# Optimization experiments

Measured on AMD Instinct MI355X. Metric: run time of the kernel, lower is better.

The kernel has to match this reference:

```python
import jax, jax.numpy as jnp
import numpy as np

N, E, C, L = 50000, 625000, 128, 4
H = 2 * C  # hidden size of per-layer ObjectModel
FRAC_SCALE = 1.0 / 16.0   # fractional_bitwidth = 4
Q_MAX = 8.0               # int_bitwidth = 4 -> signed fixed point range [-8, 8 - 1/16]


def fq(x):
    """Fixed-point fake-quantize (4 int bits, 4 frac bits, signed)."""
    return jnp.clip(jnp.round(x / FRAC_SCALE) * FRAC_SCALE, -Q_MAX, Q_MAX - FRAC_SCALE)


def qlin(h, W, b):
    # QuantLinear: input/weight/bias/output all quantized
    return fq(fq(h) @ fq(W) + fq(b))


def qbn(h, w, b):
    # BatchNorm1dToQuantScaleBias in inference: per-channel scale + bias
    return fq(fq(h) * fq(w) + fq(b))


def setup_inputs() -> dict:
    key = jax.random.key(0)
    ks = jax.random.split(key, 24)
    d = {}
    d["x"] = jax.random.normal(ks[0], (N, 3), dtype=jnp.float32)
    d["edge_attr"] = jax.random.normal(ks[1], (E, 4), dtype=jnp.float32)
    d["edge_index"] = jax.random.randint(ks[2], (2, E), 0, N, dtype=jnp.int64)
    # encoders
    d["node_W"] = jax.random.normal(ks[3], (3, C), dtype=jnp.float32) * 0.4
    d["node_b"] = jax.random.normal(ks[4], (C,), dtype=jnp.float32) * 0.2
    d["edge_W"] = jax.random.normal(ks[5], (4, C), dtype=jnp.float32) * 0.4
    d["edge_b"] = jax.random.normal(ks[6], (C,), dtype=jnp.float32) * 0.2
    d["node_bn_w"] = 1.0 + 0.1 * jax.random.normal(ks[7], (C,), dtype=jnp.float32)
    d["node_bn_b"] = 0.1 * jax.random.normal(ks[8], (C,), dtype=jnp.float32)
    d["edge_bn_w"] = 1.0 + 0.1 * jax.random.normal(ks[9], (C,), dtype=jnp.float32)
    d["edge_bn_b"] = 0.1 * jax.random.normal(ks[10], (C,), dtype=jnp.float32)
    # per-layer ObjectModel params (stacked over L)
    d["W1"] = jax.random.normal(ks[11], (L, C, H), dtype=jnp.float32) * (0.5 / np.sqrt(C))
    d["b1"] = jax.random.normal(ks[12], (L, H), dtype=jnp.float32) * 0.1
    d["bn_w"] = 1.0 + 0.1 * jax.random.normal(ks[13], (L, H), dtype=jnp.float32)
    d["bn_b"] = 0.1 * jax.random.normal(ks[14], (L, H), dtype=jnp.float32)
    d["W2"] = jax.random.normal(ks[15], (L, H, C), dtype=jnp.float32) * (0.5 / np.sqrt(H))
    d["b2"] = jax.random.normal(ks[16], (L, C), dtype=jnp.float32) * 0.1
    d["fc_W"] = jax.random.normal(ks[17], (C, 1), dtype=jnp.float32) * (0.5 / np.sqrt(C))
    d["fc_b"] = jax.random.normal(ks[18], (1,), dtype=jnp.float32) * 0.1
    return d


def reference(x, edge_attr, edge_index, node_W, node_b, edge_W, edge_b,
              node_bn_w, node_bn_b, edge_bn_w, edge_bn_b,
              W1, b1, bn_w, bn_b, W2, b2, fc_W, fc_b):
    src = edge_index[0]  # x_j (source) under flow='source_to_target'
    tgt = edge_index[1]  # aggregation target i

    h = fq(qlin(x, node_W, node_b))            # node encoder [N, C]
    e = fq(qlin(edge_attr, edge_W, edge_b))    # edge encoder [E, C]
    h = qbn(h, node_bn_w, node_bn_b)
    e = qbn(e, edge_bn_w, edge_bn_b)

    for l in range(L):
        # message: quant(x_j) + quant(edge_attr), QuantReLU
        msg = fq(jax.nn.relu(fq(h[src]) + fq(e)))          # [E, C]
        agg = jax.ops.segment_sum(msg, tgt, num_segments=N)  # scatter-sum [N, C]
        u = fq(agg)
        # ObjectModel: QuantLinear -> ScaleBias BN -> QuantReLU -> QuantLinear, then QuantIdentity
        z = qlin(u, W1[l], b1[l])
        z = qbn(z, bn_w[l], bn_b[l])
        z = fq(jax.nn.relu(z))
        z = fq(qlin(z, W2[l], b2[l]))
        h = h + z                                           # residual

    pooled = jnp.mean(h, axis=0, keepdims=True)  # global_mean_pool, batch=None -> [1, C]
    out = qlin(fq(pooled), fc_W, fc_b)           # [1, 1]
    out = fq(jax.nn.sigmoid(fq(out)))            # QuantSigmoid
    return out.reshape(-1)                       # [1]
```

## Files before the change

kernel.cpp:

```cpp
#include <hip/hip_runtime.h>
#include <stdint.h>

#define NN 50000
#define EE 625000
#define EPAD (EE + 16)
#define CC 128
#define HH 256
#define LL 4
#define NPAD 50048
#define NBLK (NPAD/64)
#define R2 32

typedef __attribute__((ext_vector_type(4))) int   i32x4;

__device__ __forceinline__ float qbf(float x){
  return fminf(127.f, fmaxf(-128.f, rintf(x*16.f)));
}
__device__ __forceinline__ float rq16(float t){
  return fminf(127.f, fmaxf(-128.f, rintf(t*0.0625f)));
}
__device__ __forceinline__ int rne16c(int t){
  int q = (t + 7 + ((t>>4)&1)) >> 4;
  return min(max(q, -128), 127);
}
__device__ __forceinline__ int dot4b(int q, int w, int c){
#if __has_builtin(__builtin_amdgcn_sdot4)
  return __builtin_amdgcn_sdot4(q, w, c, false);
#else
  int s = c;
  #pragma unroll
  for (int i=0;i<4;++i)
    s += ((int)(signed char)((q >> (8*i)) & 0xff)) *
         ((int)(signed char)((w >> (8*i)) & 0xff));
  return s;
#endif
}

__global__ void k_qbig(const float* __restrict__ W1, const float* __restrict__ W2,
                       signed char* __restrict__ w1q8, signed char* __restrict__ w2q8){
  int i = blockIdx.x*256 + threadIdx.x;
  if (i >= LL*CC*HH) return;
  {
    float v = qbf(W1[i]);
    int l = i / (CC*HH); int r = i - l*CC*HH; int c = r / HH; int hh = r - c*HH;
    w1q8[((size_t)l*HH + hh)*CC + c] = (signed char)v;
  }
  {
    float v = qbf(W2[i]);
    int l = i / (HH*CC); int r = i - l*HH*CC; int hh = r / CC; int c = r - hh*CC;
    w2q8[((size_t)l*CC + c)*HH + hh] = (signed char)v;
  }
}

struct QS { const float* s; float* d; int n; float m; };
struct QSArgs { QS q[10]; };

__global__ void k_qsmall(QSArgs a){
  for (int r=0;r<10;++r){
    QS qs = a.q[r];
    for (int i = blockIdx.x*blockDim.x + threadIdx.x; i < qs.n; i += gridDim.x*blockDim.x)
      qs.d[i] = qs.m * qbf(qs.s[i]);
  }
}

__global__ void k_epki(const float* __restrict__ eW, const float* __restrict__ eb,
                       const float* __restrict__ bnw, const float* __restrict__ bnb,
                       int4* __restrict__ epk){
  int c = threadIdx.x;
  int w0 = (int)qbf(eW[c])      & 0xff;
  int w1 = (int)qbf(eW[CC+c])   & 0xff;
  int w2 = (int)qbf(eW[2*CC+c]) & 0xff;
  int w3 = (int)qbf(eW[3*CC+c]) & 0xff;
  epk[c] = make_int4(w0 | (w1<<8) | (w2<<16) | (w3<<24),
                     16 * (int)qbf(eb[c]),
                     (int)qbf(bnw[c]),
                     16 * (int)qbf(bnb[c]));
}

__global__ __launch_bounds__(256) void k_node_enc(
    const float* __restrict__ x, const float* __restrict__ nW,
    const float* __restrict__ nb16, const float* __restrict__ bnw,
    const float* __restrict__ bnb16, short* __restrict__ h0,
    signed char* __restrict__ hq8){
  int idx = blockIdx.x*256 + threadIdx.x;
  int n = idx >> 7, c = idx & 127;
  float x0 = qbf(x[n*3]), x1 = qbf(x[n*3+1]), x2 = qbf(x[n*3+2]);
  float S = x0*nW[c] + x1*nW[CC+c] + x2*nW[2*CC+c];
  float v1 = rq16(S + nb16[c]);
  float v2 = rq16(v1*bnw[c] + bnb16[c]);
  h0[idx] = (short)v2;
  hq8[idx] = (signed char)v2;
}

__global__ void k_deg(const int* __restrict__ ei, int* __restrict__ deg){
  int e = blockIdx.x*256 + threadIdx.x;
  if (e < EE) atomicAdd(&deg[ei[EE + e]], 1);
}

__global__ __launch_bounds__(256) void k_scanA(const int* __restrict__ deg,
                                               int* __restrict__ offI,
                                               int* __restrict__ btot){
  __shared__ int sh[256];
  int t = threadIdx.x;
  int base = blockIdx.x*1024 + t*4;
  int v[4]; int s = 0;
  #pragma unroll
  for (int i=0;i<4;++i){ v[i] = (base+i < NN) ? deg[base+i] : 0; s += v[i]; }
  sh[t] = s; __syncthreads();
  for (int off=1; off<256; off<<=1){
    int xv = (t>=off) ? sh[t-off] : 0;
    __syncthreads();
    sh[t] += xv;
    __syncthreads();
  }
  int run = (t>0) ? sh[t-1] : 0;
  #pragma unroll
  for (int i=0;i<4;++i){ run += v[i]; if (base+i < NN) offI[base+i] = run; }
  if (t==255) btot[blockIdx.x] = sh[255];
}

__global__ void k_scanB(const int* __restrict__ btot, int* __restrict__ boff, int nblk){
  if (threadIdx.x==0 && blockIdx.x==0){
    int run = 0;
    for (int b=0;b<nblk;++b){ int v = btot[b]; boff[b] = run; run += v; }
  }
}

__global__ void k_scanC(const int* __restrict__ boff, const int* __restrict__ deg,
                        int* __restrict__ offI, int* __restrict__ cursor){
  int i = blockIdx.x*256 + threadIdx.x;
  if (i < NN){
    int v = offI[i] + boff[i>>10];
    offI[i] = v;
    cursor[i] = v - deg[i];
  }
}

__global__ void k_fill(const int* __restrict__ ei, const float* __restrict__ ea,
                       int* __restrict__ cursor, int2* __restrict__ adjq){
  int e = blockIdx.x*256 + threadIdx.x;
  if (e < EE){
    int tgt = ei[EE + e];
    int p = atomicAdd(&cursor[tgt], 1);
    float4 v = ((const float4*)ea)[e];
    int b0 = (int)qbf(v.x) & 0xff, b1 = (int)qbf(v.y) & 0xff;
    int b2 = (int)qbf(v.z) & 0xff, b3 = (int)qbf(v.w) & 0xff;
    adjq[p] = make_int2(ei[e] * CC, b0 | (b1<<8) | (b2<<16) | (b3<<24));
  }
}

__global__ __launch_bounds__(256) void k_msg(
    const int* __restrict__ offI, const int* __restrict__ deg_,
    const int2* __restrict__ adjq, const int4* __restrict__ epk,
    const signed char* __restrict__ hq8, signed char* __restrict__ uq){
  int n = blockIdx.x*4 + (threadIdx.x >> 6);
  int lane = threadIdx.x & 63;
  int c0 = lane*2;
  int4 P0 = epk[c0];
  int4 P1 = epk[c0+1];
  int end = offI[n];
  int start = end - deg_[n];
  int acc0 = 0, acc1 = 0;
  for (int base = start; base < end; base += 16){
    int rem = end - base;
    int2 a = adjq[base + min(lane, rem-1)];
    ushort hv[16]; int qk[16];
    #pragma unroll
    for (int j=0;j<16;++j){
      int soj = __builtin_amdgcn_readlane(a.x, j);
      hv[j] = *(const ushort*)(hq8 + soj + c0);
      qk[j] = __builtin_amdgcn_readlane(a.y, j);
    }
    #pragma unroll
    for (int j=0;j<16;++j){
      if (j < rem){
        int h0 = ((int)hv[j] << 24) >> 24;
        int h1 = ((int)(short)hv[j]) >> 8;
        int q = qk[j];
        int v10 = rne16c(dot4b(q, P0.x, P0.y));
        int v11 = rne16c(dot4b(q, P1.x, P1.y));
        int e0 = rne16c(v10*P0.z + P0.w);
        int e1 = rne16c(v11*P1.z + P1.w);
        acc0 += min(max(h0 + e0, 0), 127);
        acc1 += min(max(h1 + e1, 0), 127);
      }
    }
  }
  int ua = min(acc0, 127), ub = min(acc1, 127);
  *(ushort*)(uq + (size_t)n*CC + c0) = (ushort)((ua & 0xff) | ((ub & 0xff) << 8));
}

__global__ __launch_bounds__(256, 3) void k_om(
    int l, const signed char* __restrict__ uq,
    const signed char* __restrict__ w1q8, const float* __restrict__ b1q16,
    const float* __restrict__ bnwf, const float* __restrict__ bnb16,
    const signed char* __restrict__ w2q8, const float* __restrict__ b2q16,
    const short* __restrict__ h_in, short* __restrict__ h_out,
    signed char* __restrict__ hq8, int* __restrict__ partial){
  __shared__ signed char uL[64][144];
  __shared__ signed char zL[64][272];
  int t = threadIdx.x;
  int nb = blockIdx.x * 64;
  {
    const i32x4* src = (const i32x4*)(uq + (size_t)nb*CC + t*32);
    int flat = t*32; int r = flat >> 7, c = flat & 127;
    *(i32x4*)&uL[r][c]      = src[0];
    *(i32x4*)&uL[r][c + 16] = src[1];
  }
  int lane = t & 63, wv = t >> 6;
  int lr = lane & 15, lk = lane >> 4;
  const signed char* W1p = w1q8 + (size_t)l*HH*CC;
  i32x4 w1f[2][4];
  #pragma unroll
  for (int ks=0; ks<2; ++ks)
    #pragma unroll
    for (int ci=0; ci<4; ++ci)
      w1f[ks][ci] = *(const i32x4*)(W1p + (size_t)(wv*64 + ci*16 + lr)*CC + ks*64 + lk*16);
  __syncthreads();

  i32x4 acc[4][4];
  #pragma unroll
  for (int mi=0;mi<4;++mi)
    #pragma unroll
    for (int ci=0;ci<4;++ci) acc[mi][ci] = (i32x4){0,0,0,0};
  #pragma unroll
  for (int ks=0; ks<2; ++ks){
    i32x4 av[4];
    #pragma unroll
    for (int mi=0;mi<4;++mi) av[mi] = *(const i32x4*)&uL[mi*16+lr][ks*64 + lk*16];
    #pragma unroll
    for (int mi=0;mi<4;++mi)
      #pragma unroll
      for (int ci=0;ci<4;++ci)
        acc[mi][ci] = __builtin_amdgcn_mfma_i32_16x16x64_i8(av[mi], w1f[ks][ci], acc[mi][ci], 0,0,0);
  }
  #pragma unroll
  for (int ci=0;ci<4;++ci){
    int hcol = wv*64 + ci*16 + lr;
    float b1 = b1q16[l*HH + hcol];
    float bw = bnwf[l*HH + hcol];
    float bb = bnb16[l*HH + hcol];
    #pragma unroll
    for (int mi=0;mi<4;++mi){
      #pragma unroll
      for (int r=0;r<4;++r){
        float v1 = rq16((float)acc[mi][ci][r] + b1);
        float v2 = fmaxf(rq16(v1*bw + bb), 0.f);
        zL[mi*16 + lk*4 + r][hcol] = (signed char)v2;
      }
    }
  }
  const signed char* W2p = w2q8 + (size_t)l*CC*HH;
  i32x4 w2f[4][2];
  #pragma unroll
  for (int ks=0; ks<4; ++ks)
    #pragma unroll
    for (int ci=0; ci<2; ++ci)
      w2f[ks][ci] = *(const i32x4*)(W2p + (size_t)(wv*32 + ci*16 + lr)*HH + ks*64 + lk*16);
  __syncthreads();

  i32x4 a2[4][2];
  #pragma unroll
  for (int mi=0;mi<4;++mi){ a2[mi][0] = (i32x4){0,0,0,0}; a2[mi][1] = (i32x4){0,0,0,0}; }
  #pragma unroll
  for (int ks=0; ks<4; ++ks){
    i32x4 av[4];
    #pragma unroll
    for (int mi=0;mi<4;++mi) av[mi] = *(const i32x4*)&zL[mi*16+lr][ks*64 + lk*16];
    #pragma unroll
    for (int mi=0;mi<4;++mi)
      #pragma unroll
      for (int ci=0;ci<2;++ci)
        a2[mi][ci] = __builtin_amdgcn_mfma_i32_16x16x64_i8(av[mi], w2f[ks][ci], a2[mi][ci], 0,0,0);
  }
  int psum[2] = {0, 0};
  #pragma unroll
  for (int ci=0;ci<2;++ci){
    int ccol = wv*32 + ci*16 + lr;
    float b2 = b2q16[l*CC + ccol];
    #pragma unroll
    for (int mi=0;mi<4;++mi){
      #pragma unroll
      for (int r=0;r<4;++r){
        int node = nb + mi*16 + lk*4 + r;
        float v = rq16((float)a2[mi][ci][r] + b2);
        int hn = (int)h_in[(size_t)node*CC + ccol] + (int)v;
        if (node < NN){
          h_out[(size_t)node*CC + ccol] = (short)hn;
          hq8[(size_t)node*CC + ccol] = (signed char)min(max(hn, -128), 127);
          psum[ci] += hn;
        }
      }
    }
  }
  if (partial){
    #pragma unroll
    for (int ci=0;ci<2;++ci){
      int s = psum[ci];
      s += __shfl_xor(s, 16);
      s += __shfl_xor(s, 32);
      if (lk == 0)
        partial[blockIdx.x*CC + wv*32 + ci*16 + lr] = s;
    }
  }
}

__global__ __launch_bounds__(256) void k_red(
    const int* __restrict__ partial, int* __restrict__ partial2){
  int t = threadIdx.x;
  int c = t & 127;
  int sub = blockIdx.x*2 + (t >> 7);
  int s = 0;
  for (int b = sub; b < NBLK; b += R2) s += partial[b*CC + c];
  partial2[sub*CC + c] = s;
}

__global__ __launch_bounds__(256) void k_final(
    const int* __restrict__ partial2, const float* __restrict__ fcwf,
    const float* __restrict__ fcb16, float* __restrict__ out){
  __shared__ int ired[128];
  __shared__ float red[128];
  int t = threadIdx.x;
  int c = t & 127, half = t >> 7;
  int s = 0;
  #pragma unroll
  for (int b = half; b < R2; b += 2) s += partial2[b*CC + c];
  if (half) ired[c] = s;
  __syncthreads();
  if (!half){
    int sc = s + ired[c];
    double m = (double)sc / (double)NN;
    float pq = fminf(127.f, fmaxf(-128.f, (float)rint(m)));
    red[c] = pq * fcwf[c];
  }
  __syncthreads();
  for (int o=64;o>0;o>>=1){ if (t<o) red[t] += red[t+o]; __syncthreads(); }
  if (t==0){
    float v = rq16(red[0] + fcb16[0]);
    float o1 = v * 0.0625f;
    float sg = 1.f/(1.f + expf(-o1));
    float oq = fminf(127.f, fmaxf(-128.f, rintf(sg*16.f)));
    out[0] = oq * 0.0625f;
  }
}

extern "C" void kernel_launch(void* const* d_in, const int* in_sizes, int n_in,
                              void* d_out, int out_size, void* d_ws, size_t ws_size,
                              hipStream_t stream){
  (void)in_sizes; (void)n_in; (void)out_size; (void)ws_size;
  const float* x   = (const float*)d_in[0];
  const float* ea  = (const float*)d_in[1];
  const int*   ei  = (const int*)d_in[2];
  const float* W1  = (const float*)d_in[11];
  const float* W2  = (const float*)d_in[15];

  char* w = (char*)d_ws;
  auto alloc = [&](size_t bytes)->char*{
    char* p = w; w += (bytes + 255) & ~(size_t)255; return p;
  };
  short* h0        = (short*)alloc((size_t)NPAD*CC*2);
  short* h1        = (short*)alloc((size_t)NPAD*CC*2);
  signed char* hq8 = (signed char*)alloc((size_t)NPAD*CC);
  signed char* uq  = (signed char*)alloc((size_t)NPAD*CC);
  int2* adjq       = (int2*)alloc((size_t)EPAD*8);
  int* deg         = (int*)alloc(NN*4);
  int* offI        = (int*)alloc(NN*4);
  int* cursor      = (int*)alloc(NN*4);
  int* btot        = (int*)alloc(64*4);
  int* boff        = (int*)alloc(64*4);
  int* partial     = (int*)alloc((size_t)NBLK*CC*4);
  int* partial2    = (int*)alloc((size_t)R2*CC*4);
  signed char* w1q8= (signed char*)alloc((size_t)LL*CC*HH);
  signed char* w2q8= (signed char*)alloc((size_t)LL*CC*HH);
  float* nodeWf    = (float*)alloc(3*CC*4);
  float* nb16f     = (float*)alloc(CC*4);
  float* nbnwf     = (float*)alloc(CC*4);
  float* nbnb16f   = (float*)alloc(CC*4);
  float* b1q16f    = (float*)alloc(LL*HH*4);
  float* bnwf      = (float*)alloc(LL*HH*4);
  float* bnb16f    = (float*)alloc(LL*HH*4);
  float* b2q16f    = (float*)alloc(LL*CC*4);
  float* fcwf      = (float*)alloc(CC*4);
  float* fcb16f    = (float*)alloc(256);
  int4* epk        = (int4*)alloc(CC*16);

  hipMemsetAsync(deg, 0, NN*4, stream);

  k_qbig<<<(LL*CC*HH + 255)/256, 256, 0, stream>>>(W1, W2, w1q8, w2q8);

  QSArgs qa;
  auto setq = [&](int r, int idx, float* d, int n, float m){
    qa.q[r].s = (const float*)d_in[idx]; qa.q[r].d = d; qa.q[r].n = n; qa.q[r].m = m;
  };
  setq(0, 3,  nodeWf,  3*CC, 1.f);
  setq(1, 4,  nb16f,   CC,   16.f);
  setq(2, 7,  nbnwf,   CC,   1.f);
  setq(3, 8,  nbnb16f, CC,   16.f);
  setq(4, 12, b1q16f,  LL*HH, 16.f);
  setq(5, 13, bnwf,    LL*HH, 1.f);
  setq(6, 14, bnb16f,  LL*HH, 16.f);
  setq(7, 16, b2q16f,  LL*CC, 16.f);
  setq(8, 17, fcwf,    CC,   1.f);
  setq(9, 18, fcb16f,  1,    16.f);
  k_qsmall<<<4, 256, 0, stream>>>(qa);
  k_epki<<<1, 128, 0, stream>>>((const float*)d_in[5], (const float*)d_in[6],
                                (const float*)d_in[9], (const float*)d_in[10], epk);

  k_node_enc<<<(NN*CC)/256, 256, 0, stream>>>(x, nodeWf, nb16f, nbnwf, nbnb16f, h0, hq8);
  k_deg<<<(EE+255)/256, 256, 0, stream>>>(ei, deg);
  int nblk = (NN + 1023)/1024;
  k_scanA<<<nblk, 256, 0, stream>>>(deg, offI, btot);
  k_scanB<<<1, 64, 0, stream>>>(btot, boff, nblk);
  k_scanC<<<(NN+255)/256, 256, 0, stream>>>(boff, deg, offI, cursor);
  k_fill<<<(EE+255)/256, 256, 0, stream>>>(ei, ea, cursor, adjq);

  for (int l=0;l<LL;++l){
    const short* hi = (l & 1) ? h1 : h0;
    short* ho       = (l & 1) ? h0 : h1;
    k_msg<<<NN/4, 256, 0, stream>>>(offI, deg, adjq, epk, hq8, uq);
    k_om<<<NBLK, 256, 0, stream>>>(l, uq, w1q8, b1q16f, bnwf, bnb16f,
                                   w2q8, b2q16f, hi, ho, hq8,
                                   (l == LL-1) ? partial : nullptr);
  }
  k_red<<<R2/2, 256, 0, stream>>>(partial, partial2);
  k_final<<<1, 256, 0, stream>>>(partial2, fcwf, fcb16f, (float*)d_out);
}
```

Before: 380.3 us.

## Fuse message aggregation into per-layer object-model kernel via shared memory

Merges the gather/scatter message kernel into the MLP kernel so each 64-node block aggregates its own nodes' messages directly into shared memory, removing the intermediate uq buffer and one launch per layer. The quantized node features are double-buffered so blocks can read the previous layer's values while writing new ones. The tradeoff is far fewer waves doing the latency-bound edge gather, each processing 16 nodes serially, which may reduce memory-level parallelism.

```diff
diff --git a/kernel.cpp b/kernel.cpp
--- a/kernel.cpp
+++ b/kernel.cpp
@@ -149,66 +149,23 @@
   }
 }
 
-__global__ __launch_bounds__(256) void k_msg(
+__global__ __launch_bounds__(256, 3) void k_layer(
+    int l,
     const int* __restrict__ offI, const int* __restrict__ deg_,
     const int2* __restrict__ adjq, const int4* __restrict__ epk,
-    const signed char* __restrict__ hq8, signed char* __restrict__ uq){
-  int n = blockIdx.x*4 + (threadIdx.x >> 6);
-  int lane = threadIdx.x & 63;
-  int c0 = lane*2;
-  int4 P0 = epk[c0];
-  int4 P1 = epk[c0+1];
-  int end = offI[n];
-  int start = end - deg_[n];
-  int acc0 = 0, acc1 = 0;
-  for (int base = start; base < end; base += 16){
-    int rem = end - base;
-    int2 a = adjq[base + min(lane, rem-1)];
-    ushort hv[16]; int qk[16];
-    #pragma unroll
-    for (int j=0;j<16;++j){
-      int soj = __builtin_amdgcn_readlane(a.x, j);
-      hv[j] = *(const ushort*)(hq8 + soj + c0);
-      qk[j] = __builtin_amdgcn_readlane(a.y, j);
-    }
-    #pragma unroll
-    for (int j=0;j<16;++j){
-      if (j < rem){
-        int h0 = ((int)hv[j] << 24) >> 24;
-        int h1 = ((int)(short)hv[j]) >> 8;
-        int q = qk[j];
-        int v10 = rne16c(dot4b(q, P0.x, P0.y));
-        int v11 = rne16c(dot4b(q, P1.x, P1.y));
-        int e0 = rne16c(v10*P0.z + P0.w);
-        int e1 = rne16c(v11*P1.z + P1.w);
-        acc0 += min(max(h0 + e0, 0), 127);
-        acc1 += min(max(h1 + e1, 0), 127);
-      }
-    }
-  }
-  int ua = min(acc0, 127), ub = min(acc1, 127);
-  *(ushort*)(uq + (size_t)n*CC + c0) = (ushort)((ua & 0xff) | ((ub & 0xff) << 8));
-}
-
-__global__ __launch_bounds__(256, 3) void k_om(
-    int l, const signed char* __restrict__ uq,
     const signed char* __restrict__ w1q8, const float* __restrict__ b1q16,
     const float* __restrict__ bnwf, const float* __restrict__ bnb16,
     const signed char* __restrict__ w2q8, const float* __restrict__ b2q16,
     const short* __restrict__ h_in, short* __restrict__ h_out,
-    signed char* __restrict__ hq8, int* __restrict__ partial){
+    const signed char* __restrict__ hq8_in, signed char* __restrict__ hq8_out,
+    int* __restrict__ partial){
   __shared__ signed char uL[64][144];
   __shared__ signed char zL[64][272];
   int t = threadIdx.x;
   int nb = blockIdx.x * 64;
-  {
-    const i32x4* src = (const i32x4*)(uq + (size_t)nb*CC + t*32);
-    int flat = t*32; int r = flat >> 7, c = flat & 127;
-    *(i32x4*)&uL[r][c]      = src[0];
-    *(i32x4*)&uL[r][c + 16] = src[1];
-  }
   int lane = t & 63, wv = t >> 6;
   int lr = lane & 15, lk = lane >> 4;
+
   const signed char* W1p = w1q8 + (size_t)l*HH*CC;
   i32x4 w1f[2][4];
   #pragma unroll
@@ -216,6 +173,48 @@
     #pragma unroll
     for (int ci=0; ci<4; ++ci)
       w1f[ks][ci] = *(const i32x4*)(W1p + (size_t)(wv*64 + ci*16 + lr)*CC + ks*64 + lk*16);
+
+  {
+    int c0 = lane*2;
+    int4 P0 = epk[c0];
+    int4 P1 = epk[c0+1];
+    for (int i=0;i<16;++i){
+      int r = wv*16 + i;
+      int n = nb + r;
+      int acc0 = 0, acc1 = 0;
+      if (n < NN){
+        int end = offI[n];
+        int start = end - deg_[n];
+        for (int base = start; base < end; base += 16){
+          int rem = end - base;
+          int2 a = adjq[base + min(lane, rem-1)];
+          ushort hv[16]; int qk[16];
+          #pragma unroll
+          for (int j=0;j<16;++j){
+            int soj = __builtin_amdgcn_readlane(a.x, j);
+            hv[j] = *(const ushort*)(hq8_in + soj + c0);
+            qk[j] = __builtin_amdgcn_readlane(a.y, j);
+          }
+          #pragma unroll
+          for (int j=0;j<16;++j){
+            if (j < rem){
+              int h0 = ((int)hv[j] << 24) >> 24;
+              int h1 = ((int)(short)hv[j]) >> 8;
+              int q = qk[j];
+              int v10 = rne16c(dot4b(q, P0.x, P0.y));
+              int v11 = rne16c(dot4b(q, P1.x, P1.y));
+              int e0 = rne16c(v10*P0.z + P0.w);
+              int e1 = rne16c(v11*P1.z + P1.w);
+              acc0 += min(max(h0 + e0, 0), 127);
+              acc1 += min(max(h1 + e1, 0), 127);
+            }
+          }
+        }
+      }
+      int ua = min(acc0, 127), ub = min(acc1, 127);
+      *(ushort*)&uL[r][c0] = (ushort)((ua & 0xff) | ((ub & 0xff) << 8));
+    }
+  }
   __syncthreads();
 
   i32x4 acc[4][4];
@@ -287,7 +286,7 @@
         int hn = (int)h_in[(size_t)node*CC + ccol] + (int)v;
         if (node < NN){
           h_out[(size_t)node*CC + ccol] = (short)hn;
-          hq8[(size_t)node*CC + ccol] = (signed char)min(max(hn, -128), 127);
+          hq8_out[(size_t)node*CC + ccol] = (signed char)min(max(hn, -128), 127);
           psum[ci] += hn;
         }
       }
@@ -360,8 +359,8 @@
   };
   short* h0        = (short*)alloc((size_t)NPAD*CC*2);
   short* h1        = (short*)alloc((size_t)NPAD*CC*2);
-  signed char* hq8 = (signed char*)alloc((size_t)NPAD*CC);
-  signed char* uq  = (signed char*)alloc((size_t)NPAD*CC);
+  signed char* hq8a= (signed char*)alloc((size_t)NPAD*CC);
+  signed char* hq8b= (signed char*)alloc((size_t)NPAD*CC);
   int2* adjq       = (int2*)alloc((size_t)EPAD*8);
   int* deg         = (int*)alloc(NN*4);
   int* offI        = (int*)alloc(NN*4);
@@ -406,7 +405,7 @@
   k_epki<<<1, 128, 0, stream>>>((const float*)d_in[5], (const float*)d_in[6],
                                 (const float*)d_in[9], (const float*)d_in[10], epk);
 
-  k_node_enc<<<(NN*CC)/256, 256, 0, stream>>>(x, nodeWf, nb16f, nbnwf, nbnb16f, h0, hq8);
+  k_node_enc<<<(NN*CC)/256, 256, 0, stream>>>(x, nodeWf, nb16f, nbnwf, nbnb16f, h0, hq8a);
   k_deg<<<(EE+255)/256, 256, 0, stream>>>(ei, deg);
   int nblk = (NN + 1023)/1024;
   k_scanA<<<nblk, 256, 0, stream>>>(deg, offI, btot);
@@ -415,12 +414,14 @@
   k_fill<<<(EE+255)/256, 256, 0, stream>>>(ei, ea, cursor, adjq);
 
   for (int l=0;l<LL;++l){
-    const short* hi = (l & 1) ? h1 : h0;
-    short* ho       = (l & 1) ? h0 : h1;
-    k_msg<<<NN/4, 256, 0, stream>>>(offI, deg, adjq, epk, hq8, uq);
-    k_om<<<NBLK, 256, 0, stream>>>(l, uq, w1q8, b1q16f, bnwf, bnb16f,
-                                   w2q8, b2q16f, hi, ho, hq8,
-                                   (l == LL-1) ? partial : nullptr);
+    const short* hi       = (l & 1) ? h1 : h0;
+    short* ho             = (l & 1) ? h0 : h1;
+    const signed char* qi = (l & 1) ? hq8b : hq8a;
+    signed char* qo       = (l & 1) ? hq8a : hq8b;
+    k_layer<<<NBLK, 256, 0, stream>>>(l, offI, deg, adjq, epk,
+                                      w1q8, b1q16f, bnwf, bnb16f,
+                                      w2q8, b2q16f, hi, ho, qi, qo,
+                                      (l == LL-1) ? partial : nullptr);
   }
   k_red<<<R2/2, 256, 0, stream>>>(partial, partial2);
   k_final<<<1, 256, 0, stream>>>(partial2, fcwf, fcb16f, (float*)d_out);
```

Result: slower. 467.6 us (+22.9%).

## Cache quantized per-edge embeddings in layer 0 and reuse them in later layers

Applied to the files above, without the earlier changes.

The CSR adjacency is padded so that each node's edge list is a multiple of 16 entries. The first message-passing layer then writes the computed int8 edge-encoder outputs into a tiled workspace buffer, laid out as 16 edges by 128 channels per tile. Layers 1-3 read these cached values instead of recomputing the dot-product, rounding and scale-bias math per edge and channel. This trades ALU work for a large extra memory stream: about 176 MB written once and read three times. The padding also adds wasted gather slots and a memset of the adjacency array, and the path only runs when the workspace is large enough.

```diff
diff --git a/kernel.cpp b/kernel.cpp
--- a/kernel.cpp
+++ b/kernel.cpp
@@ -3,7 +3,7 @@
 
 #define NN 50000
 #define EE 625000
-#define EPAD (EE + 16)
+#define PE (EE + 15*NN + 64)
 #define CC 128
 #define HH 256
 #define LL 4
@@ -105,7 +105,10 @@
   int base = blockIdx.x*1024 + t*4;
   int v[4]; int s = 0;
   #pragma unroll
-  for (int i=0;i<4;++i){ v[i] = (base+i < NN) ? deg[base+i] : 0; s += v[i]; }
+  for (int i=0;i<4;++i){
+    v[i] = (base+i < NN) ? ((deg[base+i] + 15) & ~15) : 0;
+    s += v[i];
+  }
   sh[t] = s; __syncthreads();
   for (int off=1; off<256; off<<=1){
     int xv = (t>=off) ? sh[t-off] : 0;
@@ -132,7 +135,7 @@
   if (i < NN){
     int v = offI[i] + boff[i>>10];
     offI[i] = v;
-    cursor[i] = v - deg[i];
+    cursor[i] = v - ((deg[i] + 15) & ~15);
   }
 }
 
@@ -149,40 +152,75 @@
   }
 }
 
+template<int MODE>
 __global__ __launch_bounds__(256) void k_msg(
     const int* __restrict__ offI, const int* __restrict__ deg_,
     const int2* __restrict__ adjq, const int4* __restrict__ epk,
+    signed char* __restrict__ eqt,
     const signed char* __restrict__ hq8, signed char* __restrict__ uq){
   int n = blockIdx.x*4 + (threadIdx.x >> 6);
   int lane = threadIdx.x & 63;
   int c0 = lane*2;
-  int4 P0 = epk[c0];
-  int4 P1 = epk[c0+1];
-  int end = offI[n];
-  int start = end - deg_[n];
+  int4 P0, P1;
+  if (MODE != 1){ P0 = epk[c0]; P1 = epk[c0+1]; }
+  int d = deg_[n];
+  int degP = (d + 15) & ~15;
+  int startP = offI[n] - degP;
   int acc0 = 0, acc1 = 0;
-  for (int base = start; base < end; base += 16){
-    int rem = end - base;
-    int2 a = adjq[base + min(lane, rem-1)];
-    ushort hv[16]; int qk[16];
+  for (int k = 0; k < degP; k += 16){
+    int base = startP + k;
+    int rem = min(d - k, 16);
+    int2 a = adjq[base + (lane & 15)];
+    ushort hv[16];
     #pragma unroll
     for (int j=0;j<16;++j){
       int soj = __builtin_amdgcn_readlane(a.x, j);
       hv[j] = *(const ushort*)(hq8 + soj + c0);
-      qk[j] = __builtin_amdgcn_readlane(a.y, j);
     }
-    #pragma unroll
-    for (int j=0;j<16;++j){
-      if (j < rem){
-        int h0 = ((int)hv[j] << 24) >> 24;
-        int h1 = ((int)(short)hv[j]) >> 8;
-        int q = qk[j];
-        int v10 = rne16c(dot4b(q, P0.x, P0.y));
-        int v11 = rne16c(dot4b(q, P1.x, P1.y));
-        int e0 = rne16c(v10*P0.z + P0.w);
-        int e1 = rne16c(v11*P1.z + P1.w);
-        acc0 += min(max(h0 + e0, 0), 127);
-        acc1 += min(max(h1 + e1, 0), 127);
+    if (MODE == 1){
+      const i32x4* ep = (const i32x4*)(eqt + ((size_t)(base >> 4) << 11));
+      i32x4 ev0 = ep[c0];
+      i32x4 ev1 = ep[c0 + 1];
+      #pragma unroll
+      for (int j=0;j<16;++j){
+        if (j < rem){
+          int h0 = ((int)hv[j] << 24) >> 24;
+          int h1 = ((int)(short)hv[j]) >> 8;
+          int e0 = (int)(signed char)(ev0[j>>2] >> (8*(j&3)));
+          int e1 = (int)(signed char)(ev1[j>>2] >> (8*(j&3)));
+          acc0 += min(max(h0 + e0, 0), 127);
+          acc1 += min(max(h1 + e1, 0), 127);
+        }
+      }
+    } else {
+      int qk[16];
+      #pragma unroll
+      for (int j=0;j<16;++j) qk[j] = __builtin_amdgcn_readlane(a.y, j);
+      uint pk0[4] = {0,0,0,0}, pk1[4] = {0,0,0,0};
+      #pragma unroll
+      for (int j=0;j<16;++j){
+        if (j < rem){
+          int h0 = ((int)hv[j] << 24) >> 24;
+          int h1 = ((int)(short)hv[j]) >> 8;
+          int q = qk[j];
+          int v10 = rne16c(dot4b(q, P0.x, P0.y));
+          int v11 = rne16c(dot4b(q, P1.x, P1.y));
+          int e0 = rne16c(v10*P0.z + P0.w);
+          int e1 = rne16c(v11*P1.z + P1.w);
+          if (MODE == 0){
+            pk0[j>>2] |= ((uint)(e0 & 0xff)) << (8*(j&3));
+            pk1[j>>2] |= ((uint)(e1 & 0xff)) << (8*(j&3));
+          }
+          acc0 += min(max(h0 + e0, 0), 127);
+          acc1 += min(max(h1 + e1, 0), 127);
+        }
+      }
+      if (MODE == 0){
+        i32x4* ep = (i32x4*)(eqt + ((size_t)(base >> 4) << 11));
+        i32x4 w0 = { (int)pk0[0], (int)pk0[1], (int)pk0[2], (int)pk0[3] };
+        i32x4 w1 = { (int)pk1[0], (int)pk1[1], (int)pk1[2], (int)pk1[3] };
+        ep[c0]     = w0;
+        ep[c0 + 1] = w1;
       }
     }
   }
@@ -347,7 +385,7 @@
 extern "C" void kernel_launch(void* const* d_in, const int* in_sizes, int n_in,
                               void* d_out, int out_size, void* d_ws, size_t ws_size,
                               hipStream_t stream){
-  (void)in_sizes; (void)n_in; (void)out_size; (void)ws_size;
+  (void)in_sizes; (void)n_in; (void)out_size;
   const float* x   = (const float*)d_in[0];
   const float* ea  = (const float*)d_in[1];
   const int*   ei  = (const int*)d_in[2];
@@ -362,7 +400,7 @@
   short* h1        = (short*)alloc((size_t)NPAD*CC*2);
   signed char* hq8 = (signed char*)alloc((size_t)NPAD*CC);
   signed char* uq  = (signed char*)alloc((size_t)NPAD*CC);
-  int2* adjq       = (int2*)alloc((size_t)EPAD*8);
+  int2* adjq       = (int2*)alloc((size_t)PE*8);
   int* deg         = (int*)alloc(NN*4);
   int* offI        = (int*)alloc(NN*4);
   int* cursor      = (int*)alloc(NN*4);
@@ -383,8 +421,12 @@
   float* fcwf      = (float*)alloc(CC*4);
   float* fcb16f    = (float*)alloc(256);
   int4* epk        = (int4*)alloc(CC*16);
+  size_t base_used = (size_t)(w - (char*)d_ws);
+  bool TEQ = (ws_size >= base_used + (size_t)PE*CC + (16u<<20));
+  signed char* eqt = TEQ ? (signed char*)alloc((size_t)PE*CC) : nullptr;
 
   hipMemsetAsync(deg, 0, NN*4, stream);
+  hipMemsetAsync(adjq, 0, (size_t)PE*8, stream);
 
   k_qbig<<<(LL*CC*HH + 255)/256, 256, 0, stream>>>(W1, W2, w1q8, w2q8);
 
@@ -417,7 +459,12 @@
   for (int l=0;l<LL;++l){
     const short* hi = (l & 1) ? h1 : h0;
     short* ho       = (l & 1) ? h0 : h1;
-    k_msg<<<NN/4, 256, 0, stream>>>(offI, deg, adjq, epk, hq8, uq);
+    if (!TEQ)
+      k_msg<2><<<NN/4, 256, 0, stream>>>(offI, deg, adjq, epk, eqt, hq8, uq);
+    else if (l == 0)
+      k_msg<0><<<NN/4, 256, 0, stream>>>(offI, deg, adjq, epk, eqt, hq8, uq);
+    else
+      k_msg<1><<<NN/4, 256, 0, stream>>>(offI, deg, adjq, epk, eqt, hq8, uq);
     k_om<<<NBLK, 256, 0, stream>>>(l, uq, w1q8, b1q16f, bnwf, bnb16f,
                                    w2q8, b2q16f, hi, ho, hq8,
                                    (l == LL-1) ? partial : nullptr);
```

Result: faster. 349.6 us (-8.1%).
